# Optimization experiments

Measured on AMD Instinct MI355X. Metric: run time of the kernel, lower is better.

## Reference

```python
import jax, jax.numpy as jnp
import numpy as np

N_A = 3
N_CLS = 80
IGNORE_THRE = 0.6
EPS = 1e-7


def _pairwise_iou_cxcywh(a, b):
    # a: [..., M, 4], b: [..., N, 4] in (cx, cy, w, h) -> IoU [..., M, N]
    a_xy, a_wh = a[..., :, None, :2], a[..., :, None, 2:4]
    b_xy, b_wh = b[..., None, :, :2], b[..., None, :, 2:4]
    tl = jnp.maximum(a_xy - a_wh * 0.5, b_xy - b_wh * 0.5)
    br = jnp.minimum(a_xy + a_wh * 0.5, b_xy + b_wh * 0.5)
    inter = jnp.prod(jnp.clip(br - tl, 0.0), axis=-1)
    area_a = a_wh[..., 0] * a_wh[..., 1]
    area_b = b_wh[..., 0] * b_wh[..., 1]
    return inter / jnp.maximum(area_a + area_b - inter, 1e-16)


def _bce(p, t):
    p = jnp.clip(p, EPS, 1.0 - EPS)
    return -(t * jnp.log(p) + (1.0 - t) * jnp.log(1.0 - p))


def _yolo_loss(raw, labels, anchors_all, anchor_indices, img_size):
    nB = raw.shape[0]
    nG = raw.shape[2]
    nCH = 5 + N_CLS
    K = labels.shape[1]
    sg = jax.lax.stop_gradient

    # decode raw: (B, A*CH, G, G) -> (B, A, G, G, CH)
    raw = jnp.transpose(raw.reshape(nB, N_A, nCH, nG, nG), (0, 1, 3, 4, 2))
    xy_offset = jax.nn.sigmoid(raw[..., 0:2])            # (B,A,G,G,2)
    wh_scale = raw[..., 2:4]                             # (B,A,G,G,2)
    conf = jax.nn.sigmoid(raw[..., 4])                   # (B,A,G,G)
    classes = jax.nn.sigmoid(raw[..., 5:])               # (B,A,G,G,ncls)

    anchors = anchors_all[anchor_indices]                # (3,2), pixels
    g = jnp.arange(nG, dtype=raw.dtype)
    xs = g[None, None, None, :]
    ys = g[None, None, :, None]

    # detached decoded predictions, normalized to [0,1]
    px = (sg(xy_offset[..., 0]) + xs) / nG
    py = (sg(xy_offset[..., 1]) + ys) / nG
    pw = jnp.minimum(jnp.exp(sg(wh_scale[..., 0])) * anchors[:, 0][None, :, None, None] / img_size, 1.0)
    ph = jnp.minimum(jnp.exp(sg(wh_scale[..., 1])) * anchors[:, 1][None, :, None, None] / img_size, 1.0)
    pred_boxes = jnp.stack([px, py, pw, ph], axis=-1).reshape(nB, -1, 4)  # (B, A*G*G, 4)

    # labels: (B, K, 5) = [cls, xc, yc, w, h]; targets are constants
    labels = sg(labels)
    nlabel = jnp.sum(jnp.sum(labels, axis=2) > 0, axis=1)                 # (B,)
    valid_k = jnp.arange(K)[None, :] < nlabel[:, None]                    # (B,K)
    tcls = labels[..., 0].astype(jnp.int32)
    tx = labels[..., 1] * nG
    ty = labels[..., 2] * nG
    tw = labels[..., 3]
    th = labels[..., 4]
    ti = tx.astype(jnp.int32)
    tj = ty.astype(jnp.int32)

    # anchor matching on centered (0,0,w,h) boxes against all 9 anchors
    anch00 = jnp.concatenate([jnp.zeros_like(anchors_all), anchors_all / img_size], axis=1)  # (9,4)
    gt00 = jnp.stack([jnp.zeros_like(tw), jnp.zeros_like(tw), tw, th], axis=-1)              # (B,K,4)
    a_ious = _pairwise_iou_cxcywh(gt00, anch00[None])                                        # (B,K,9)
    best_n_all = jnp.argmax(a_ious, axis=-1)                                                 # (B,K)
    valid_anchor = jnp.any(best_n_all[..., None] == anchor_indices[None, None, :], axis=-1)
    valid = valid_k & valid_anchor                                                           # (B,K)
    best_n = best_n_all % N_A

    # ignore mask: preds whose best IoU against any (valid) gt exceeds threshold
    gt_boxes = jnp.stack([tx / nG, ty / nG, tw, th], axis=-1) * valid_k[..., None].astype(raw.dtype)
    pred_ious = _pairwise_iou_cxcywh(pred_boxes, gt_boxes)               # (B, A*G*G, K)
    ignore = (jnp.max(pred_ious, axis=-1) > IGNORE_THRE).reshape(nB, N_A, nG, nG)
    penalty_mask = ~ignore

    # scatter gt assignments; invalid rows dropped via OOB batch index
    b_idx = jnp.broadcast_to(jnp.arange(nB)[:, None], (nB, K))
    b_s = jnp.where(valid, b_idx, nB)

    obj_mask = jnp.zeros((nB, N_A, nG, nG), dtype=bool).at[b_s, best_n, tj, ti].set(True, mode='drop')
    penalty_mask = penalty_mask.at[b_s, best_n, tj, ti].set(True, mode='drop')

    naw = anchors / img_size                                             # (3,2)
    tgt_vals = jnp.stack([
        tx - jnp.floor(tx),
        ty - jnp.floor(ty),
        jnp.log(tw / naw[best_n, 0] + 1e-16),
        jnp.log(th / naw[best_n, 1] + 1e-16),
    ], axis=-1)                                                          # (B,K,4)
    target4 = jnp.zeros((nB, N_A, nG, nG, 4), raw.dtype).at[b_s, best_n, tj, ti].set(tgt_vals, mode='drop')
    tgt_scale = jnp.zeros((nB, N_A, nG, nG), raw.dtype).at[b_s, best_n, tj, ti].set(
        jnp.sqrt(2.0 - tw * th), mode='drop')
    tcls_oh = jnp.zeros((nB, N_A, nG, nG, N_CLS), raw.dtype).at[b_s, best_n, tj, ti, tcls].set(1.0, mode='drop')

    obj_f = obj_mask.astype(raw.dtype)
    pen_f = penalty_mask.astype(raw.dtype)
    w2 = tgt_scale * tgt_scale                                           # (B,A,G,G)

    loss_xy = jnp.sum(obj_f[..., None] * w2[..., None] * _bce(xy_offset, target4[..., 0:2]))
    loss_wh = jnp.sum(obj_f[..., None] * w2[..., None] * jnp.square(wh_scale - target4[..., 2:4]))
    loss_obj = jnp.sum(pen_f * _bce(conf, obj_f))
    loss_cls = jnp.sum(obj_f[..., None] * _bce(classes, tcls_oh))
    return loss_xy + 0.5 * loss_wh + loss_obj + loss_cls


def setup_inputs() -> dict:
    key = jax.random.key(0)
    k1, k2, k3, k4 = jax.random.split(key, 4)
    nB, K, nG = 16, 50, 76
    raw = jax.random.normal(k1, (nB, N_A * (5 + N_CLS), nG, nG), jnp.float32) * 0.5
    cls = jax.random.randint(k2, (nB, K), 0, N_CLS).astype(jnp.float32)
    xy = jax.random.uniform(k3, (nB, K, 2), jnp.float32, 0.02, 0.98)
    wh = jax.random.uniform(k4, (nB, K, 2), jnp.float32, 0.02, 0.4)
    labels = jnp.concatenate([cls[..., None], xy, wh], axis=-1)
    # make per-image label counts < K (rows of zeros are "no label")
    labels = labels * (jnp.arange(K) < 40).astype(jnp.float32)[None, :, None]
    anchors_all = jnp.array([[10, 13], [16, 30], [33, 23], [30, 61], [62, 45],
                             [59, 119], [116, 90], [156, 198], [373, 326]], jnp.float32)
    anchor_indices = jnp.array([0, 1, 2], jnp.int32)
    return {"raw": raw, "labels": labels, "anchors_all": anchors_all,
            "anchor_indices": anchor_indices, "img_size": 608}


def reference(raw, labels, anchors_all, anchor_indices, img_size):
    return _yolo_loss(raw, labels, anchors_all, anchor_indices, img_size)
```

## Files before the change

### kernel.cpp

```cpp
#include <hip/hip_runtime.h>
#include <math.h>

#define NB   16
#define KL   50
#define NG   76
#define NA   3
#define NCLS 80
#define NCH  85
#define GG   (NG*NG)
#define CELLS (NA*GG)
#define CPT  4
#define TPB  64
#define CPB  (TPB*CPT)
#define LOSS_BX ((CELLS + CPB - 1) / CPB)
#define NPART (LOSS_BX * NB)

__device__ __forceinline__ float softplusf(float x) {
    float t = __expf(-fabsf(x));
    return fmaxf(x, 0.0f) + __logf(1.0f + t);
}

__global__ __launch_bounds__(64) void yolo_fused(
    const float* __restrict__ raw,
    const float* __restrict__ labels,
    const float* __restrict__ anchors_all,
    const int*   __restrict__ anchor_indices,
    const int*   __restrict__ img_size_p,
    float* __restrict__ partials)
{
    const int b = blockIdx.y;

    __shared__ float4 s_box[KL];
    __shared__ float  s_c[KL];
    __shared__ int    s_meta[KL];
    __shared__ float4 s_tgt[KL];
    __shared__ float  s_w2[KL];
    __shared__ int    s_tc[KL];

    const float img = (float)img_size_p[0];
    const float inv_img = __builtin_amdgcn_rcpf(img);

    {
        const int k = threadIdx.x;
        int has = 0;
        float cls = 0.f, tx = 0.f, ty = 0.f, tw = 0.f, th = 0.f;
        if (k < KL) {
            const float* L = labels + ((size_t)b * KL + k) * 5;
            cls = L[0];
            tw = L[3]; th = L[4];
            has = ((cls + L[1] + L[2] + tw + th) > 0.0f) ? 1 : 0;
            tx = L[1] * (float)NG;
            ty = L[2] * (float)NG;
        }
        unsigned long long bal = __ballot(has);
        int nlabel = __popcll(bal);

        if (k < KL) {
            int valid_k = (k < nlabel) ? 1 : 0;

            float best = -1.0f; int bestn = 0;
            float area_t = tw * th;
            for (int n = 0; n < 9; ++n) {
                float aw = anchors_all[2 * n + 0] * inv_img;
                float ah = anchors_all[2 * n + 1] * inv_img;
                float inter = fmaxf(fminf(tw, aw), 0.0f) * fmaxf(fminf(th, ah), 0.0f);
                float iou = inter / fmaxf(area_t + aw * ah - inter, 1e-16f);
                if (iou > best) { best = iou; bestn = n; }
            }
            int va = 0;
            for (int t = 0; t < 3; ++t) va |= (bestn == anchor_indices[t]) ? 1 : 0;
            int bn = bestn % NA;
            int ti = (int)tx, tj = (int)ty;
            int valid = valid_k && va && (ti >= 0) && (ti < NG) && (tj >= 0) && (tj < NG);
            s_meta[k] = valid ? (bn * GG + tj * NG + ti) : -1;

            float vkf = valid_k ? 1.0f : 0.0f;
            float gx = tx * (1.0f / (float)NG) * vkf;
            float gy = ty * (1.0f / (float)NG) * vkf;
            float gw = tw * vkf, gh = th * vkf;
            s_box[k] = make_float4(gx - 0.5f * gw, gy - 0.5f * gh,
                                   gx + 0.5f * gw, gy + 0.5f * gh);
            s_c[k] = 0.375f * (gw * gh);

            float naw = anchors_all[anchor_indices[bn] * 2 + 0] * inv_img;
            float nah = anchors_all[anchor_indices[bn] * 2 + 1] * inv_img;
            s_tgt[k] = make_float4(tx - floorf(tx), ty - floorf(ty),
                                   __logf(tw / naw + 1e-16f),
                                   __logf(th / nah + 1e-16f));
            s_w2[k] = 2.0f - tw * th;
            s_tc[k] = (int)cls;
        }
    }
    __syncthreads();

    const int c0 = blockIdx.x * CPB + threadIdx.x * CPT;
    const bool live = c0 < CELLS;
    const int cb = live ? c0 : 0;

    const int a = cb / GG;
    const int r = cb - a * GG;
    const int j = r / NG;
    const int i = r - j * NG;
    const float* R = raw + ((size_t)(b * NA + a) * NCH) * GG + r;

    float4 rx4 = *(const float4*)(R);
    float4 ry4 = *(const float4*)(R + GG);
    float4 rw4 = *(const float4*)(R + 2 * GG);
    float4 rh4 = *(const float4*)(R + 3 * GG);
    float4 rc4 = *(const float4*)(R + 4 * GG);

    int ai = anchor_indices[a];
    float aw = anchors_all[2 * ai + 0] * inv_img;
    float ah = anchors_all[2 * ai + 1] * inv_img;

    float rxv[CPT] = {rx4.x, rx4.y, rx4.z, rx4.w};
    float ryv[CPT] = {ry4.x, ry4.y, ry4.z, ry4.w};
    float rwv[CPT] = {rw4.x, rw4.y, rw4.z, rw4.w};
    float rhv[CPT] = {rh4.x, rh4.y, rh4.z, rh4.w};
    float rcv[CPT] = {rc4.x, rc4.y, rc4.z, rc4.w};

    float ax0[CPT], ax1[CPT], ay0[CPT], ay1[CPT], tA[CPT], margin[CPT];
    int kobj[CPT];
    #pragma unroll
    for (int cc = 0; cc < CPT; ++cc) {
        float sx = __builtin_amdgcn_rcpf(1.0f + __expf(-rxv[cc]));
        float sy = __builtin_amdgcn_rcpf(1.0f + __expf(-ryv[cc]));
        float px = (sx + (float)(i + cc)) * (1.0f / (float)NG);
        float py = (sy + (float)j) * (1.0f / (float)NG);
        float pw = fminf(__expf(rwv[cc]) * aw, 1.0f);
        float ph = fminf(__expf(rhv[cc]) * ah, 1.0f);
        tA[cc] = 0.375f * (pw * ph);
        ax0[cc] = px - 0.5f * pw; ax1[cc] = px + 0.5f * pw;
        ay0[cc] = py - 0.5f * ph; ay1[cc] = py + 0.5f * ph;
        margin[cc] = -1.0f;
        kobj[cc] = -1;
    }

    #pragma unroll 5
    for (int k = 0; k < KL; ++k) {
        float4 g = s_box[k];
        float cB = s_c[k];
        int   mk = s_meta[k];
        #pragma unroll
        for (int cc = 0; cc < CPT; ++cc) {
            float iw = fminf(ax1[cc], g.z) - fmaxf(ax0[cc], g.x);
            float ih = fminf(ay1[cc], g.w) - fmaxf(ay0[cc], g.y);
            float inter = fmaxf(iw, 0.0f) * fmaxf(ih, 0.0f);
            margin[cc] = fmaxf(margin[cc], inter - cB);
            kobj[cc] = (mk == cb + cc) ? k : kobj[cc];
        }
    }

    float loss = 0.0f;
    #pragma unroll
    for (int cc = 0; cc < CPT; ++cc) {
        bool ignore = margin[cc] > tA[cc];
        bool obj = kobj[cc] >= 0;

        if (obj || !ignore)
            loss += softplusf(rcv[cc]) - (obj ? rcv[cc] : 0.0f);

        if (obj) {
            float4 t = s_tgt[kobj[cc]];
            float w2 = s_w2[kobj[cc]];
            loss += w2 * ((softplusf(rxv[cc]) - t.x * rxv[cc]) +
                          (softplusf(ryv[cc]) - t.y * ryv[cc]));
            float dw = rwv[cc] - t.z, dh = rhv[cc] - t.w;
            loss += 0.5f * w2 * (dw * dw + dh * dh);
            int tc = s_tc[kobj[cc]];
            float cl = 0.0f;
            #pragma unroll 8
            for (int ch = 0; ch < NCLS; ++ch) {
                float z = R[(5 + ch) * GG + cc];
                cl += softplusf(z);
                if (ch == tc) cl -= z;
            }
            loss += cl;
        }
    }
    if (!live) loss = 0.0f;

    for (int off = 32; off > 0; off >>= 1)
        loss += __shfl_down(loss, off, 64);
    if (threadIdx.x == 0)
        partials[(size_t)b * LOSS_BX + blockIdx.x] = loss;
}

__global__ __launch_bounds__(256) void yolo_finalize(
    const float* __restrict__ partials, float* __restrict__ out)
{
    float s = 0.0f;
    for (int i = threadIdx.x; i < NPART; i += 256) s += partials[i];
    for (int off = 32; off > 0; off >>= 1)
        s += __shfl_down(s, off, 64);
    __shared__ float red[4];
    if ((threadIdx.x & 63) == 0) red[threadIdx.x >> 6] = s;
    __syncthreads();
    if (threadIdx.x == 0) out[0] = red[0] + red[1] + red[2] + red[3];
}

extern "C" void kernel_launch(void* const* d_in, const int* in_sizes, int n_in,
                              void* d_out, int out_size, void* d_ws, size_t ws_size,
                              hipStream_t stream) {
    const float* raw            = (const float*)d_in[0];
    const float* labels         = (const float*)d_in[1];
    const float* anchors_all    = (const float*)d_in[2];
    const int*   anchor_indices = (const int*)d_in[3];
    const int*   img_size_p     = (const int*)d_in[4];
    float* out = (float*)d_out;

    float* partials = (float*)d_ws;

    dim3 grid(LOSS_BX, NB);
    yolo_fused<<<grid, TPB, 0, stream>>>(raw, labels, anchors_all,
                                         anchor_indices, img_size_p, partials);
    yolo_finalize<<<1, 256, 0, stream>>>(partials, out);
}
```

Measured before the change: 146.8 us.

## Use 256-thread blocks with 2 cells per thread, early raw loads, label-count loop bound

Each thread now handles 2 cells instead of 4, and each block has 256 threads instead of 64, so block and wave parallelism change. The raw channel loads are issued before the label preprocessing so their latency overlaps the setup and the barrier. The IoU loop now stops at the actual label count instead of the fixed maximum, which skips the padded zero labels. Per-block reduction goes through shared memory across four waves, at the cost of an extra barrier.

```diff
diff --git a/kernel.cpp b/kernel.cpp
--- a/kernel.cpp
+++ b/kernel.cpp
@@ -9,8 +9,8 @@
 #define NCH  85
 #define GG   (NG*NG)
 #define CELLS (NA*GG)
-#define CPT  4
-#define TPB  64
+#define CPT  2
+#define TPB  256
 #define CPB  (TPB*CPT)
 #define LOSS_BX ((CELLS + CPB - 1) / CPB)
 #define NPART (LOSS_BX * NB)
@@ -20,7 +20,7 @@
     return fmaxf(x, 0.0f) + __logf(1.0f + t);
 }
 
-__global__ __launch_bounds__(64) void yolo_fused(
+__global__ __launch_bounds__(256) void yolo_fused(
     const float* __restrict__ raw,
     const float* __restrict__ labels,
     const float* __restrict__ anchors_all,
@@ -36,11 +36,29 @@
     __shared__ float4 s_tgt[KL];
     __shared__ float  s_w2[KL];
     __shared__ int    s_tc[KL];
+    __shared__ int    s_nl;
+    __shared__ float  s_red[4];
 
     const float img = (float)img_size_p[0];
     const float inv_img = __builtin_amdgcn_rcpf(img);
 
-    {
+    const int c0 = blockIdx.x * CPB + threadIdx.x * CPT;
+    const bool live = c0 < CELLS;
+    const int cb = live ? c0 : 0;
+
+    const int a = cb / GG;
+    const int r = cb - a * GG;
+    const int j = r / NG;
+    const int i = r - j * NG;
+    const float* R = raw + ((size_t)(b * NA + a) * NCH) * GG + r;
+
+    float2 rx2 = *(const float2*)(R);
+    float2 ry2 = *(const float2*)(R + GG);
+    float2 rw2 = *(const float2*)(R + 2 * GG);
+    float2 rh2 = *(const float2*)(R + 3 * GG);
+    float2 rc2 = *(const float2*)(R + 4 * GG);
+
+    if (threadIdx.x < 64) {
         const int k = threadIdx.x;
         int has = 0;
         float cls = 0.f, tx = 0.f, ty = 0.f, tw = 0.f, th = 0.f;
@@ -54,6 +72,7 @@
         }
         unsigned long long bal = __ballot(has);
         int nlabel = __popcll(bal);
+        if (k == 0) s_nl = nlabel;
 
         if (k < KL) {
             int valid_k = (k < nlabel) ? 1 : 0;
@@ -92,32 +111,17 @@
         }
     }
     __syncthreads();
-
-    const int c0 = blockIdx.x * CPB + threadIdx.x * CPT;
-    const bool live = c0 < CELLS;
-    const int cb = live ? c0 : 0;
-
-    const int a = cb / GG;
-    const int r = cb - a * GG;
-    const int j = r / NG;
-    const int i = r - j * NG;
-    const float* R = raw + ((size_t)(b * NA + a) * NCH) * GG + r;
-
-    float4 rx4 = *(const float4*)(R);
-    float4 ry4 = *(const float4*)(R + GG);
-    float4 rw4 = *(const float4*)(R + 2 * GG);
-    float4 rh4 = *(const float4*)(R + 3 * GG);
-    float4 rc4 = *(const float4*)(R + 4 * GG);
+    const int nl = s_nl;
 
     int ai = anchor_indices[a];
     float aw = anchors_all[2 * ai + 0] * inv_img;
     float ah = anchors_all[2 * ai + 1] * inv_img;
 
-    float rxv[CPT] = {rx4.x, rx4.y, rx4.z, rx4.w};
-    float ryv[CPT] = {ry4.x, ry4.y, ry4.z, ry4.w};
-    float rwv[CPT] = {rw4.x, rw4.y, rw4.z, rw4.w};
-    float rhv[CPT] = {rh4.x, rh4.y, rh4.z, rh4.w};
-    float rcv[CPT] = {rc4.x, rc4.y, rc4.z, rc4.w};
+    float rxv[CPT] = {rx2.x, rx2.y};
+    float ryv[CPT] = {ry2.x, ry2.y};
+    float rwv[CPT] = {rw2.x, rw2.y};
+    float rhv[CPT] = {rh2.x, rh2.y};
+    float rcv[CPT] = {rc2.x, rc2.y};
 
     float ax0[CPT], ax1[CPT], ay0[CPT], ay1[CPT], tA[CPT], margin[CPT];
     int kobj[CPT];
@@ -137,7 +141,7 @@
     }
 
     #pragma unroll 5
-    for (int k = 0; k < KL; ++k) {
+    for (int k = 0; k < nl; ++k) {
         float4 g = s_box[k];
         float cB = s_c[k];
         int   mk = s_meta[k];
@@ -182,8 +186,11 @@
 
     for (int off = 32; off > 0; off >>= 1)
         loss += __shfl_down(loss, off, 64);
+    if ((threadIdx.x & 63) == 0) s_red[threadIdx.x >> 6] = loss;
+    __syncthreads();
     if (threadIdx.x == 0)
-        partials[(size_t)b * LOSS_BX + blockIdx.x] = loss;
+        partials[(size_t)b * LOSS_BX + blockIdx.x] =
+            s_red[0] + s_red[1] + s_red[2] + s_red[3];
 }
 
 __global__ __launch_bounds__(256) void yolo_finalize(
```

Result: faster. 140.3 us (-4.4%).
